# Optimization experiments

Hardware: AMD Instinct MI355X
Metric: run time of the kernel (lower is better)

The kernel has to match this reference:

```python
import jax, jax.numpy as jnp
import numpy as np

N = 50000   # num nodes
E = 800000  # num edges (avg degree 16)
D = 128     # in = hidden = out channels


def setup_inputs() -> dict:
    key = jax.random.key(0)
    k0, k1, k2, k3, k4, k5 = jax.random.split(key, 6)
    x = jax.random.normal(k0, (N, D), dtype=jnp.float32)
    edge_index = jax.random.randint(k1, (2, E), 0, N, dtype=jnp.int32)
    scale = 1.0 / np.sqrt(D)
    W1 = jax.random.normal(k2, (D, D), dtype=jnp.float32) * scale
    b1 = jax.random.normal(k3, (D,), dtype=jnp.float32) * 0.01
    W2 = jax.random.normal(k4, (D, D), dtype=jnp.float32) * scale
    b2 = jax.random.normal(k5, (D,), dtype=jnp.float32) * 0.01
    return {"x": x, "edge_index": edge_index, "W1": W1, "b1": b1, "W2": W2, "b2": b2}


def reference(x, edge_index, W1, b1, W2, b2):
    n = x.shape[0]
    src, dst = edge_index[0], edge_index[1]
    # GCN adds self-loops before normalization
    loops = jnp.arange(n, dtype=src.dtype)
    s = jnp.concatenate([src, loops])
    d = jnp.concatenate([dst, loops])
    # symmetric normalization: deg^{-1/2}[s] * deg^{-1/2}[d]
    deg = jax.ops.segment_sum(jnp.ones_like(d, dtype=x.dtype), d, num_segments=n)
    dinv = jnp.where(deg > 0, jax.lax.rsqrt(deg), 0.0)
    ew = dinv[s] * dinv[d]  # [E+N]

    def gcn_conv(h, W, b):
        h = h @ W                                   # [N, D] dense transform first
        msg = ew[:, None] * h[s]                     # gather over edges [E+N, D]
        agg = jax.ops.segment_sum(msg, d, num_segments=n)  # scatter-add [N, D]
        return agg + b

    # layer 1: conv -> Identity BN -> ELU (dropout=0.0 -> no-op)
    h = jax.nn.elu(gcn_conv(x, W1, b1))
    # layer 2 (last): conv -> Identity BN -> ELU
    out = jax.nn.elu(gcn_conv(h, W2, b2))
    return out
```

## Files before the change

### kernel.cpp

```cpp
#include <hip/hip_runtime.h>
#include <math.h>

#define D 128
#define BCAP 8192
#define SLICE 64
#define PB 256

typedef __attribute__((ext_vector_type(8))) short bf16x8;
typedef __attribute__((ext_vector_type(4))) float f32x4;


__device__ inline float2 bf2f2(unsigned int u) {
    union { unsigned int i; float f; } a, b;
    a.i = u << 16;
    b.i = u & 0xffff0000u;
    return make_float2(a.f, b.f);
}

__device__ inline unsigned short f2bf(float f) {
    union { float f; unsigned int i; } u;
    u.f = f;
    unsigned int r = u.i + 0x7fffu + ((u.i >> 16) & 1u);
    return (unsigned short)(r >> 16);
}


__global__ __launch_bounds__(256) void k1_part_convw(
        const int* __restrict__ src, const int* __restrict__ dst,
        const float* __restrict__ W1, const float* __restrict__ W2,
        unsigned short* __restrict__ Wt1, unsigned short* __restrict__ Wt2,
        unsigned int* __restrict__ pairs, unsigned char* __restrict__ cellCnt,
        int e, int chunk) {
    const int tid = threadIdx.x;
    if ((int)blockIdx.x >= PB) {
        int i = ((int)blockIdx.x - PB) * 256 + tid;
        int which = i >> 14;
        int idx = i & 16383;
        int k = idx >> 7, n = idx & 127;
        const float* W = which ? W2 : W1;
        unsigned short* Wt = which ? Wt2 : Wt1;
        Wt[n * 128 + k] = f2bf(W[k * 128 + n]);
        return;
    }
    __shared__ int cur[256];
    const int j = blockIdx.x;
    cur[tid] = 0;
    __syncthreads();
    const int e0 = j * chunk;
    const int e1 = min(e0 + chunk, e);
    for (int i = e0 + tid; i < e1; i += 256) {
        int d = dst[i], s = src[i];
        int b = d >> 8;
        int off = atomicAdd(&cur[b], 1);
        if (off < SLICE)
            pairs[((size_t)(j * 256 + b)) * SLICE + off] =
                (unsigned int)s | ((unsigned int)(d & 255) << 16);
    }
    __syncthreads();
    cellCnt[j * 256 + tid] = (unsigned char)min(cur[tid], SLICE);
}


__device__ __forceinline__ void gemm_body(unsigned short (*Ws)[136], int gbid,
                                          const void* __restrict__ Ain, int a_fp32,
                                          const unsigned short* __restrict__ Wt,
                                          unsigned int* __restrict__ Cb, int N) {
    const int tid = threadIdx.x;
    {
        int n = tid >> 1;
        int kb = (tid & 1) * 64;
        const uint4* g = (const uint4*)(Wt + (size_t)n * 128 + kb);
        uint4* s = (uint4*)&Ws[n][kb];
#pragma unroll
        for (int j = 0; j < 8; ++j) s[j] = g[j];
    }

    const int wid = tid >> 6;
    const int lane = tid & 63;
    const int quad = lane >> 4;
    const int ln = lane & 15;
    const int m = gbid * 64 + wid * 16 + ln;
    const bool valid = (m < N);

    f32x4 acc[8];
#pragma unroll
    for (int c = 0; c < 8; ++c) acc[c] = (f32x4){0.f, 0.f, 0.f, 0.f};

    __syncthreads();

#pragma unroll
    for (int ks = 0; ks < 4; ++ks) {
        const int k0 = ks * 32;
        bf16x8 af;
        if (a_fp32) {
            const float* A = (const float*)Ain;
            float4 lo = make_float4(0.f, 0.f, 0.f, 0.f), hi = lo;
            if (valid) {
                lo = *(const float4*)&A[(size_t)m * 128 + k0 + quad * 8];
                hi = *(const float4*)&A[(size_t)m * 128 + k0 + quad * 8 + 4];
            }
            af[0] = (short)f2bf(lo.x); af[1] = (short)f2bf(lo.y);
            af[2] = (short)f2bf(lo.z); af[3] = (short)f2bf(lo.w);
            af[4] = (short)f2bf(hi.x); af[5] = (short)f2bf(hi.y);
            af[6] = (short)f2bf(hi.z); af[7] = (short)f2bf(hi.w);
        } else {
            const uint4* A4 = (const uint4*)Ain;
            uint4 v = valid ? A4[(size_t)m * 16 + ks * 4 + quad]
                            : make_uint4(0u, 0u, 0u, 0u);
            union { uint4 u; bf16x8 h; } cv;
            cv.u = v;
            af = cv.h;
        }
#pragma unroll
        for (int c = 0; c < 8; ++c) {
            bf16x8 bf = *(const bf16x8*)&Ws[c * 16 + ln][k0 + quad * 8];
            acc[c] = __builtin_amdgcn_mfma_f32_16x16x32_bf16(af, bf, acc[c], 0, 0, 0);
        }
    }

    const int rowbase = gbid * 64 + wid * 16 + quad * 4;
#pragma unroll
    for (int c = 0; c < 8; ++c) {
#pragma unroll
        for (int r = 0; r < 4; ++r) {
            float v = acc[c][r];
            float vn = __shfl_xor(v, 1);
            int grow = rowbase + r;
            if (!(ln & 1) && grow < N) {
                unsigned int u = (unsigned int)f2bf(v) | ((unsigned int)f2bf(vn) << 16);
                Cb[(size_t)grow * 64 + c * 8 + (ln >> 1)] = u;
            }
        }
    }
}


__global__ __launch_bounds__(256) void k2_gemm_partB(
        const void* __restrict__ Ain, const unsigned short* __restrict__ Wt,
        unsigned int* __restrict__ Cb, int N, int gemmBlocks,
        const unsigned int* __restrict__ pairs, const unsigned char* __restrict__ cellCnt,
        unsigned short* __restrict__ col, unsigned int* __restrict__ meta,
        float* __restrict__ dinv, int n) {
    __shared__ __align__(16) unsigned char smem[128 * 136 * 2];
    const int tid = threadIdx.x;

    if ((int)blockIdx.x < gemmBlocks) {
        gemm_body((unsigned short(*)[136])smem, blockIdx.x, Ain, 1, Wt, Cb, N);
        return;
    }

    int* deg = (int*)smem;
    int* sc  = deg + 256;
    int* cur = sc + 256;
    const int b = blockIdx.x - gemmBlocks;

    deg[tid] = 0;
    __syncthreads();

    const int c = cellCnt[tid * 256 + b];
    const unsigned int* cell = pairs + ((size_t)(tid * 256 + b)) * SLICE;
    for (int q = 0; q < c; ++q) atomicAdd(&deg[cell[q] >> 16], 1);
    __syncthreads();

    int v = deg[tid];
    sc[tid] = v;
    __syncthreads();
    for (int o = 1; o < 256; o <<= 1) {
        int t = (tid >= o) ? sc[tid - o] : 0;
        __syncthreads();
        sc[tid] += t;
        __syncthreads();
    }
    int startw = sc[tid] - v;
    cur[tid] = startw;

    int node = b * 256 + tid;
    if (node < n) {
        meta[node] = ((unsigned int)(b * BCAP + startw) << 10) | (unsigned int)v;
        dinv[node] = rsqrtf((float)(v + 1));
    }
    __syncthreads();

    for (int q = 0; q < c; ++q) {
        unsigned int p = cell[q];
        int dl = p >> 16;
        int off = atomicAdd(&cur[dl], 1);
        col[(size_t)b * BCAP + off] = (unsigned short)(p & 0xffffu);
    }
}


__global__ __launch_bounds__(256) void gemm_mfma(const void* __restrict__ Ain,
                                                 const unsigned short* __restrict__ Wt,
                                                 unsigned int* __restrict__ Cb, int N) {
    __shared__ __align__(16) unsigned short Ws[128][136];
    gemm_body(Ws, blockIdx.x, Ain, 0, Wt, Cb, N);
}


__global__ __launch_bounds__(256) void agg_elu(const unsigned int* __restrict__ hb,
                                               const unsigned int* __restrict__ meta,
                                               const unsigned short* __restrict__ col,
                                               const float* __restrict__ dinv,
                                               const float* __restrict__ bias,
                                               float* __restrict__ outf,
                                               unsigned int* __restrict__ outb,
                                               int write_bf, int n) {
    const int wid = threadIdx.x >> 6;
    const int lane = threadIdx.x & 63;
    const int node = blockIdx.x * 4 + wid;
    if (node >= n) return;

    const float di = dinv[node];
    float2 self = bf2f2(hb[(size_t)node * 64 + lane]);
    float2 a0 = make_float2(di * self.x, di * self.y);
    float2 a1 = make_float2(0.f, 0.f), a2 = make_float2(0.f, 0.f),
           a3 = make_float2(0.f, 0.f), a4 = make_float2(0.f, 0.f),
           a5 = make_float2(0.f, 0.f), a6 = make_float2(0.f, 0.f),
           a7 = make_float2(0.f, 0.f);

    const unsigned int m = meta[node];
    const int s0 = (int)(m >> 10);
    const int s1 = s0 + (int)(m & 1023u);
    int i = s0;
    for (; i + 8 <= s1; i += 8) {
        int c0 = col[i + 0], c1 = col[i + 1], c2 = col[i + 2], c3 = col[i + 3];
        int c4 = col[i + 4], c5 = col[i + 5], c6 = col[i + 6], c7 = col[i + 7];
        float w0 = dinv[c0], w1 = dinv[c1], w2 = dinv[c2], w3 = dinv[c3];
        float w4 = dinv[c4], w5 = dinv[c5], w6 = dinv[c6], w7 = dinv[c7];
        unsigned int u0 = hb[(size_t)c0 * 64 + lane];
        unsigned int u1 = hb[(size_t)c1 * 64 + lane];
        unsigned int u2 = hb[(size_t)c2 * 64 + lane];
        unsigned int u3 = hb[(size_t)c3 * 64 + lane];
        unsigned int u4 = hb[(size_t)c4 * 64 + lane];
        unsigned int u5 = hb[(size_t)c5 * 64 + lane];
        unsigned int u6 = hb[(size_t)c6 * 64 + lane];
        unsigned int u7 = hb[(size_t)c7 * 64 + lane];
        float2 v0 = bf2f2(u0), v1 = bf2f2(u1), v2 = bf2f2(u2), v3 = bf2f2(u3);
        float2 v4 = bf2f2(u4), v5 = bf2f2(u5), v6 = bf2f2(u6), v7 = bf2f2(u7);
        a0.x = fmaf(w0, v0.x, a0.x); a0.y = fmaf(w0, v0.y, a0.y);
        a1.x = fmaf(w1, v1.x, a1.x); a1.y = fmaf(w1, v1.y, a1.y);
        a2.x = fmaf(w2, v2.x, a2.x); a2.y = fmaf(w2, v2.y, a2.y);
        a3.x = fmaf(w3, v3.x, a3.x); a3.y = fmaf(w3, v3.y, a3.y);
        a4.x = fmaf(w4, v4.x, a4.x); a4.y = fmaf(w4, v4.y, a4.y);
        a5.x = fmaf(w5, v5.x, a5.x); a5.y = fmaf(w5, v5.y, a5.y);
        a6.x = fmaf(w6, v6.x, a6.x); a6.y = fmaf(w6, v6.y, a6.y);
        a7.x = fmaf(w7, v7.x, a7.x); a7.y = fmaf(w7, v7.y, a7.y);
    }
    for (; i < s1; ++i) {
        int c = col[i];
        float ww = dinv[c];
        float2 v = bf2f2(hb[(size_t)c * 64 + lane]);
        a0.x = fmaf(ww, v.x, a0.x); a0.y = fmaf(ww, v.y, a0.y);
    }

    float2 bv = ((const float2*)bias)[lane];
    float sx = (a0.x + a1.x) + (a2.x + a3.x) + (a4.x + a5.x) + (a6.x + a7.x);
    float sy = (a0.y + a1.y) + (a2.y + a3.y) + (a4.y + a5.y) + (a6.y + a7.y);
    float rx = fmaf(di, sx, bv.x);
    float ry = fmaf(di, sy, bv.y);
    rx = rx > 0.0f ? rx : expm1f(rx);
    ry = ry > 0.0f ? ry : expm1f(ry);
    if (write_bf) {
        outb[(size_t)node * 64 + lane] =
            (unsigned int)f2bf(rx) | ((unsigned int)f2bf(ry) << 16);
    } else {
        ((float2*)outf)[(size_t)node * 64 + lane] = make_float2(rx, ry);
    }
}


extern "C" void kernel_launch(void* const* d_in, const int* in_sizes, int n_in,
                              void* d_out, int out_size, void* d_ws, size_t ws_size,
                              hipStream_t stream) {
    const float* x  = (const float*)d_in[0];
    const int*   ei = (const int*)d_in[1];
    const float* W1 = (const float*)d_in[2];
    const float* b1 = (const float*)d_in[3];
    const float* W2 = (const float*)d_in[4];
    const float* b2 = (const float*)d_in[5];
    float* out = (float*)d_out;

    const int N = in_sizes[0] / D;
    const int E = in_sizes[1] / 2;
    const int* src = ei;
    const int* dst = ei + E;
    const int NB = (N + 255) / 256;

    char* ws = (char*)d_ws;
    size_t off = 0;
    auto alloc = [&](size_t bytes) -> void* {
        void* p = ws + off;
        off = (off + bytes + 255) & ~(size_t)255;
        return p;
    };
    unsigned int*   pairs   = (unsigned int*)alloc((size_t)PB * 256 * SLICE * 4);
    unsigned char*  cellCnt = (unsigned char*)alloc((size_t)PB * 256);
    unsigned short* col     = (unsigned short*)alloc((size_t)NB * BCAP * 2);
    unsigned int*   meta    = (unsigned int*)alloc((size_t)N * 4);
    float*          dinv    = (float*)alloc((size_t)N * 4);
    unsigned short* Wt1     = (unsigned short*)alloc(128 * 128 * 2);
    unsigned short* Wt2     = (unsigned short*)alloc(128 * 128 * 2);
    unsigned int*   hb      = (unsigned int*)alloc((size_t)N * 64 * 4);
    unsigned int*   g1      = (unsigned int*)alloc((size_t)N * 64 * 4);
    (void)ws_size; (void)n_in; (void)out_size;

    const int chunk = (E + PB - 1) / PB;
    const int gemmBlocks = (N + 63) / 64;
    const int aggBlocks = (N + 3) / 4;

    k1_part_convw<<<PB + 128, 256, 0, stream>>>(src, dst, W1, W2, Wt1, Wt2,
                                                pairs, cellCnt, E, chunk);
    k2_gemm_partB<<<gemmBlocks + NB, 256, 0, stream>>>(x, Wt1, hb, N, gemmBlocks,
                                                       pairs, cellCnt, col, meta, dinv, N);
    agg_elu<<<aggBlocks, 256, 0, stream>>>(hb, meta, col, dinv, b1, nullptr, g1, 1, N);
    gemm_mfma<<<gemmBlocks, 256, 0, stream>>>(g1, Wt2, hb, N);
    agg_elu<<<aggBlocks, 256, 0, stream>>>(hb, meta, col, dinv, b2, out, nullptr, 0, N);
}
```

Before: 205.5 us.

## Fuse layer-1 aggregation with layer-2 GEMM and reshuffle kernel stages

Layer-1 aggregation+ELU now writes a 16-node tile into shared memory, and the same block immediately runs the W2 MFMA on it. This removes the g1 round trip through global memory and one kernel launch. The edge partition, W1 transpose and first GEMM move into a single kernel, where each GEMM block converts W1 to bf16 itself. The CSR build (partB) becomes its own kernel. The costs are redundant W1 conversion in every GEMM block, re-streaming Wt2 for every 16-node tile, and lower MFMA utilisation per block.

```diff
diff --git a/kernel.cpp b/kernel.cpp
--- a/kernel.cpp
+++ b/kernel.cpp
@@ -25,56 +25,10 @@
 }
 
 
-__global__ __launch_bounds__(256) void k1_part_convw(
-        const int* __restrict__ src, const int* __restrict__ dst,
-        const float* __restrict__ W1, const float* __restrict__ W2,
-        unsigned short* __restrict__ Wt1, unsigned short* __restrict__ Wt2,
-        unsigned int* __restrict__ pairs, unsigned char* __restrict__ cellCnt,
-        int e, int chunk) {
-    const int tid = threadIdx.x;
-    if ((int)blockIdx.x >= PB) {
-        int i = ((int)blockIdx.x - PB) * 256 + tid;
-        int which = i >> 14;
-        int idx = i & 16383;
-        int k = idx >> 7, n = idx & 127;
-        const float* W = which ? W2 : W1;
-        unsigned short* Wt = which ? Wt2 : Wt1;
-        Wt[n * 128 + k] = f2bf(W[k * 128 + n]);
-        return;
-    }
-    __shared__ int cur[256];
-    const int j = blockIdx.x;
-    cur[tid] = 0;
-    __syncthreads();
-    const int e0 = j * chunk;
-    const int e1 = min(e0 + chunk, e);
-    for (int i = e0 + tid; i < e1; i += 256) {
-        int d = dst[i], s = src[i];
-        int b = d >> 8;
-        int off = atomicAdd(&cur[b], 1);
-        if (off < SLICE)
-            pairs[((size_t)(j * 256 + b)) * SLICE + off] =
-                (unsigned int)s | ((unsigned int)(d & 255) << 16);
-    }
-    __syncthreads();
-    cellCnt[j * 256 + tid] = (unsigned char)min(cur[tid], SLICE);
-}
-
-
-__device__ __forceinline__ void gemm_body(unsigned short (*Ws)[136], int gbid,
+__device__ __forceinline__ void gemm_core(unsigned short (*Ws)[136], int gbid,
                                           const void* __restrict__ Ain, int a_fp32,
-                                          const unsigned short* __restrict__ Wt,
                                           unsigned int* __restrict__ Cb, int N) {
     const int tid = threadIdx.x;
-    {
-        int n = tid >> 1;
-        int kb = (tid & 1) * 64;
-        const uint4* g = (const uint4*)(Wt + (size_t)n * 128 + kb);
-        uint4* s = (uint4*)&Ws[n][kb];
-#pragma unroll
-        for (int j = 0; j < 8; ++j) s[j] = g[j];
-    }
-
     const int wid = tid >> 6;
     const int lane = tid & 63;
     const int quad = lane >> 4;
@@ -135,24 +89,57 @@
 }
 
 
-__global__ __launch_bounds__(256) void k2_gemm_partB(
-        const void* __restrict__ Ain, const unsigned short* __restrict__ Wt,
-        unsigned int* __restrict__ Cb, int N, int gemmBlocks,
-        const unsigned int* __restrict__ pairs, const unsigned char* __restrict__ cellCnt,
-        unsigned short* __restrict__ col, unsigned int* __restrict__ meta,
-        float* __restrict__ dinv, int n) {
+__global__ __launch_bounds__(256) void k1_all(
+        const int* __restrict__ src, const int* __restrict__ dst,
+        const float* __restrict__ x, const float* __restrict__ W1,
+        const float* __restrict__ W2, unsigned short* __restrict__ Wt2,
+        unsigned int* __restrict__ pairs, unsigned char* __restrict__ cellCnt,
+        unsigned int* __restrict__ hb1, int e, int chunk, int N, int gemmBlocks) {
     __shared__ __align__(16) unsigned char smem[128 * 136 * 2];
     const int tid = threadIdx.x;
-
-    if ((int)blockIdx.x < gemmBlocks) {
-        gemm_body((unsigned short(*)[136])smem, blockIdx.x, Ain, 1, Wt, Cb, N);
-        return;
-    }
-
-    int* deg = (int*)smem;
-    int* sc  = deg + 256;
-    int* cur = sc + 256;
-    const int b = blockIdx.x - gemmBlocks;
+    const int bid = blockIdx.x;
+
+    if (bid < PB) {
+        int* cur = (int*)smem;
+        cur[tid] = 0;
+        __syncthreads();
+        const int e0 = bid * chunk;
+        const int e1 = min(e0 + chunk, e);
+        for (int i = e0 + tid; i < e1; i += 256) {
+            int d = dst[i], s = src[i];
+            int b = d >> 8;
+            int off = atomicAdd(&cur[b], 1);
+            if (off < SLICE)
+                pairs[((size_t)(bid * 256 + b)) * SLICE + off] =
+                    (unsigned int)s | ((unsigned int)(d & 255) << 16);
+        }
+        __syncthreads();
+        cellCnt[bid * 256 + tid] = (unsigned char)min(cur[tid], SLICE);
+    } else if (bid < PB + gemmBlocks) {
+        unsigned short (*Ws)[136] = (unsigned short(*)[136])smem;
+        for (int j = 0; j < 64; ++j) {
+            int idx = tid + j * 256;
+            Ws[idx & 127][idx >> 7] = f2bf(W1[idx]);
+        }
+        gemm_core(Ws, bid - PB, x, 1, hb1, N);
+    } else {
+        int i = (bid - PB - gemmBlocks) * 256 + tid;
+        int k = i >> 7, n = i & 127;
+        Wt2[n * 128 + k] = f2bf(W2[i]);
+    }
+}
+
+
+__global__ __launch_bounds__(256) void partB(const unsigned int* __restrict__ pairs,
+                                             const unsigned char* __restrict__ cellCnt,
+                                             unsigned short* __restrict__ col,
+                                             unsigned int* __restrict__ meta,
+                                             float* __restrict__ dinv, int n) {
+    __shared__ int deg[256];
+    __shared__ int sc[256];
+    __shared__ int cur[256];
+    const int b = blockIdx.x;
+    const int tid = threadIdx.x;
 
     deg[tid] = 0;
     __syncthreads();
@@ -190,27 +177,11 @@
 }
 
 
-__global__ __launch_bounds__(256) void gemm_mfma(const void* __restrict__ Ain,
-                                                 const unsigned short* __restrict__ Wt,
-                                                 unsigned int* __restrict__ Cb, int N) {
-    __shared__ __align__(16) unsigned short Ws[128][136];
-    gemm_body(Ws, blockIdx.x, Ain, 0, Wt, Cb, N);
-}
-
-
-__global__ __launch_bounds__(256) void agg_elu(const unsigned int* __restrict__ hb,
-                                               const unsigned int* __restrict__ meta,
-                                               const unsigned short* __restrict__ col,
-                                               const float* __restrict__ dinv,
-                                               const float* __restrict__ bias,
-                                               float* __restrict__ outf,
-                                               unsigned int* __restrict__ outb,
-                                               int write_bf, int n) {
-    const int wid = threadIdx.x >> 6;
-    const int lane = threadIdx.x & 63;
-    const int node = blockIdx.x * 4 + wid;
-    if (node >= n) return;
-
+__device__ __forceinline__ float2 agg_node(const unsigned int* __restrict__ hb,
+                                           const unsigned int* __restrict__ meta,
+                                           const unsigned short* __restrict__ col,
+                                           const float* __restrict__ dinv,
+                                           int node, int lane, float2 bv) {
     const float di = dinv[node];
     float2 self = bf2f2(hb[(size_t)node * 64 + lane]);
     float2 a0 = make_float2(di * self.x, di * self.y);
@@ -254,19 +225,91 @@
         a0.x = fmaf(ww, v.x, a0.x); a0.y = fmaf(ww, v.y, a0.y);
     }
 
-    float2 bv = ((const float2*)bias)[lane];
     float sx = (a0.x + a1.x) + (a2.x + a3.x) + (a4.x + a5.x) + (a6.x + a7.x);
     float sy = (a0.y + a1.y) + (a2.y + a3.y) + (a4.y + a5.y) + (a6.y + a7.y);
     float rx = fmaf(di, sx, bv.x);
     float ry = fmaf(di, sy, bv.y);
     rx = rx > 0.0f ? rx : expm1f(rx);
     ry = ry > 0.0f ? ry : expm1f(ry);
-    if (write_bf) {
-        outb[(size_t)node * 64 + lane] =
-            (unsigned int)f2bf(rx) | ((unsigned int)f2bf(ry) << 16);
-    } else {
-        ((float2*)outf)[(size_t)node * 64 + lane] = make_float2(rx, ry);
-    }
+    return make_float2(rx, ry);
+}
+
+
+__global__ __launch_bounds__(256) void k3_agg_gemm(
+        const unsigned int* __restrict__ hb1, const unsigned int* __restrict__ meta,
+        const unsigned short* __restrict__ col, const float* __restrict__ dinv,
+        const float* __restrict__ b1, const unsigned short* __restrict__ Wt2,
+        unsigned int* __restrict__ hb2, int n) {
+    __shared__ unsigned int g1s[16 * 68];
+    __shared__ __align__(16) unsigned short Ws[64][136];
+
+    const int tid = threadIdx.x;
+    const int wid = tid >> 6;
+    const int lane = tid & 63;
+    const int nodeBase = blockIdx.x * 16;
+    const float2 bv = ((const float2*)b1)[lane];
+
+    for (int t = 0; t < 4; ++t) {
+        const int node = nodeBase + wid * 4 + t;
+        unsigned int packed = 0;
+        if (node < n) {
+            float2 r = agg_node(hb1, meta, col, dinv, node, lane, bv);
+            packed = (unsigned int)f2bf(r.x) | ((unsigned int)f2bf(r.y) << 16);
+        }
+        g1s[(wid * 4 + t) * 68 + lane] = packed;
+    }
+    __syncthreads();
+
+    const int quad = lane >> 4;
+    const int ln = lane & 15;
+
+#pragma unroll
+    for (int pass = 0; pass < 2; ++pass) {
+        {
+            int nloc = tid >> 2;
+            int kb = (tid & 3) * 32;
+            const uint4* g = (const uint4*)(Wt2 + (size_t)(pass * 64 + nloc) * 128 + kb);
+            uint4* s = (uint4*)&Ws[nloc][kb];
+            s[0] = g[0]; s[1] = g[1]; s[2] = g[2]; s[3] = g[3];
+        }
+        __syncthreads();
+
+        f32x4 acc = (f32x4){0.f, 0.f, 0.f, 0.f};
+#pragma unroll
+        for (int ks = 0; ks < 4; ++ks) {
+            bf16x8 af = *(const bf16x8*)&g1s[ln * 68 + ks * 16 + quad * 4];
+            bf16x8 bf = *(const bf16x8*)&Ws[wid * 16 + ln][ks * 32 + quad * 8];
+            acc = __builtin_amdgcn_mfma_f32_16x16x32_bf16(af, bf, acc, 0, 0, 0);
+        }
+        const int c = pass * 4 + wid;
+#pragma unroll
+        for (int r = 0; r < 4; ++r) {
+            float v = acc[r];
+            float vn = __shfl_xor(v, 1);
+            int grow = nodeBase + quad * 4 + r;
+            if (!(ln & 1) && grow < n) {
+                hb2[(size_t)grow * 64 + c * 8 + (ln >> 1)] =
+                    (unsigned int)f2bf(v) | ((unsigned int)f2bf(vn) << 16);
+            }
+        }
+        __syncthreads();
+    }
+}
+
+
+__global__ __launch_bounds__(256) void agg_elu(const unsigned int* __restrict__ hb,
+                                               const unsigned int* __restrict__ meta,
+                                               const unsigned short* __restrict__ col,
+                                               const float* __restrict__ dinv,
+                                               const float* __restrict__ bias,
+                                               float* __restrict__ outf, int n) {
+    const int wid = threadIdx.x >> 6;
+    const int lane = threadIdx.x & 63;
+    const int node = blockIdx.x * 4 + wid;
+    if (node >= n) return;
+    const float2 bv = ((const float2*)bias)[lane];
+    float2 r = agg_node(hb, meta, col, dinv, node, lane, bv);
+    ((float2*)outf)[(size_t)node * 64 + lane] = r;
 }
 
 
@@ -299,21 +342,18 @@
     unsigned short* col     = (unsigned short*)alloc((size_t)NB * BCAP * 2);
     unsigned int*   meta    = (unsigned int*)alloc((size_t)N * 4);
     float*          dinv    = (float*)alloc((size_t)N * 4);
-    unsigned short* Wt1     = (unsigned short*)alloc(128 * 128 * 2);
     unsigned short* Wt2     = (unsigned short*)alloc(128 * 128 * 2);
-    unsigned int*   hb      = (unsigned int*)alloc((size_t)N * 64 * 4);
-    unsigned int*   g1      = (unsigned int*)alloc((size_t)N * 64 * 4);
+    unsigned int*   hb1     = (unsigned int*)alloc((size_t)N * 64 * 4);
+    unsigned int*   hb2     = (unsigned int*)alloc((size_t)N * 64 * 4);
     (void)ws_size; (void)n_in; (void)out_size;
 
     const int chunk = (E + PB - 1) / PB;
     const int gemmBlocks = (N + 63) / 64;
-    const int aggBlocks = (N + 3) / 4;
-
-    k1_part_convw<<<PB + 128, 256, 0, stream>>>(src, dst, W1, W2, Wt1, Wt2,
-                                                pairs, cellCnt, E, chunk);
-    k2_gemm_partB<<<gemmBlocks + NB, 256, 0, stream>>>(x, Wt1, hb, N, gemmBlocks,
-                                                       pairs, cellCnt, col, meta, dinv, N);
-    agg_elu<<<aggBlocks, 256, 0, stream>>>(hb, meta, col, dinv, b1, nullptr, g1, 1, N);
-    gemm_mfma<<<gemmBlocks, 256, 0, stream>>>(g1, Wt2, hb, N);
-    agg_elu<<<aggBlocks, 256, 0, stream>>>(hb, meta, col, dinv, b2, out, nullptr, 0, N);
-}
+
+    k1_all<<<PB + gemmBlocks + 64, 256, 0, stream>>>(src, dst, x, W1, W2, Wt2,
+                                                     pairs, cellCnt, hb1, E, chunk,
+                                                     N, gemmBlocks);
+    partB<<<NB, 256, 0, stream>>>(pairs, cellCnt, col, meta, dinv, N);
+    k3_agg_gemm<<<(N + 15) / 16, 256, 0, stream>>>(hb1, meta, col, dinv, b1, Wt2, hb2, N);
+    agg_elu<<<(N + 3) / 4, 256, 0, stream>>>(hb2, meta, col, dinv, b2, out, N);
+}
```

After: 198.6 us (median of 2 runs). 3.3% less time.
